# Performance work log

Hardware: AMD Instinct MI355X
Metric: run time of the kernel (lower is better)

The kernel has to match this reference:

```python
import jax, jax.numpy as jnp
import numpy as np

H, TD, NUM_NODES = 128, 32, 256
B, N, T = 16, 256, 128


def sinusoidal_pe(t, h, dtype=jnp.float32):
    pos = jnp.arange(t, dtype=dtype)[:, None]                      # [T,1]
    div = jnp.exp(jnp.arange(0, h, 2, dtype=dtype) * (-np.log(10000.0) / h))
    pe = jnp.zeros((t, h), dtype=dtype)
    pe = pe.at[:, 0::2].set(jnp.sin(pos * div))
    pe = pe.at[:, 1::2].set(jnp.cos(pos * div))
    return pe                                                      # [T,H]


def setup_inputs() -> dict:
    key = jax.random.key(0)
    ks = jax.random.split(key, 20)
    lin = lambda k, i, o: jax.random.normal(k, (i, o), jnp.float32) / np.sqrt(i)
    return {
        "xf": jax.random.normal(ks[0], (B, N, T, H), jnp.float32),
        "ex": jax.random.normal(ks[1], (B, T, TD), jnp.float32),
        "nf": jax.random.randint(ks[2], (N,), 0, NUM_NODES),
        "mask": jax.random.randint(ks[3], (B, N, T, H), 0, 2).astype(bool),
        "W_in": lin(ks[4], 3 * H, H), "b_in": jnp.zeros((H,), jnp.float32),
        "W_t": lin(ks[5], TD, H), "b_t": jnp.zeros((H,), jnp.float32),
        "E_node": jax.random.normal(ks[6], (NUM_NODES, H), jnp.float32),
        "W_q": lin(ks[7], H, H), "b_q": jnp.zeros((H,), jnp.float32),
        "W_k": lin(ks[8], H, H), "b_k": jnp.zeros((H,), jnp.float32),
        "W_v": lin(ks[9], H, H), "b_v": jnp.zeros((H,), jnp.float32),
        "W_o": lin(ks[10], H, H), "b_o": jnp.zeros((H,), jnp.float32),
    }


def reference(xf, ex, nf, mask, W_in, b_in, W_t, b_t, E_node,
              W_q, b_q, W_k, b_k, W_v, b_v, W_o, b_o):
    b, n, t, h = xf.shape
    # pos-embed + concat(time, node embeds) + linear + GELU (exact erf, like torch F.gelu)
    pe = sinusoidal_pe(t, h, xf.dtype)                              # [T,H]
    time_e = (ex @ W_t + b_t)[:, None, :, :]                        # [B,1,T,H]
    node_e = E_node[nf][None, :, None, :]                           # [1,N,1,H]
    cat = jnp.concatenate([
        xf + pe,
        jnp.broadcast_to(time_e, (b, n, t, h)),
        jnp.broadcast_to(node_e, (b, n, t, h)),
    ], axis=-1)                                                     # [B,N,T,3H]
    x = jax.nn.gelu(cat @ W_in + b_in, approximate=False)           # [B,N,T,H]
    # attention over T per (B,N)
    q = x @ W_q + b_q
    k = x @ W_k + b_k
    v = x @ W_v + b_v
    scores = jnp.einsum('bnsh,bnth->bnst', q, k) * (1.0 / np.sqrt(h))
    A = jnp.nan_to_num(jax.nn.softmax(scores, axis=-1), nan=0.0)    # [B,N,T,T]
    # masked-confidence reduction (detached A in original)
    t_masking = jnp.all(mask, axis=-1)[:, :, None, :].astype(A.dtype)  # [B,N,1,T]
    conf = 1.0 - jnp.sum(jax.lax.stop_gradient(A) * t_masking, axis=-1)  # [B,N,T]
    rec = jnp.einsum('bnst,bnth->bnsh', A, v)                       # [B,N,T,H]
    rec = rec @ W_o + b_o
    return rec, conf
```

## Files before the change

### kernel.cpp

```cpp
#include <hip/hip_runtime.h>
#include <hip/hip_bf16.h>
#include <stdint.h>


typedef __bf16 bf16;
typedef __bf16 bf16x4 __attribute__((ext_vector_type(4)));
typedef __bf16 bf16x8 __attribute__((ext_vector_type(8)));
typedef float  f32x4  __attribute__((ext_vector_type(4)));

#define MFMA16(a, b, c) __builtin_amdgcn_mfma_f32_16x16x32_bf16((a), (b), (c), 0, 0, 0)

__device__ __forceinline__ int allBytesNonzero(unsigned v) {
    return ((v - 0x01010101u) & ~v & 0x80808080u) == 0u;
}

__device__ __forceinline__ bf16x8 cvt8(const float* p) {
    float4 f0 = *reinterpret_cast<const float4*>(p);
    float4 f1 = *reinterpret_cast<const float4*>(p + 4);
    bf16x8 r;
    r[0] = (bf16)f0.x; r[1] = (bf16)f0.y; r[2] = (bf16)f0.z; r[3] = (bf16)f0.w;
    r[4] = (bf16)f1.x; r[5] = (bf16)f1.y; r[6] = (bf16)f1.z; r[7] = (bf16)f1.w;
    return r;
}

__device__ __forceinline__ float gelu_erf(float v) {
    float x  = v * 0.70710678118654752f;
    float ax = fabsf(x);
    float t  = __builtin_amdgcn_rcpf(1.0f + 0.3275911f * ax);
    float p  = ((((1.061405429f * t - 1.453152027f) * t + 1.421413741f) * t
                 - 0.284496736f) * t + 0.254829592f) * t;
    float er = 1.0f - p * __expf(-ax * ax);
    er = copysignf(er, x);
    return 0.5f * v * (1.0f + er);
}

__global__ void prep_all(const float* __restrict__ W_in, const float* __restrict__ Wq,
                         const float* __restrict__ Wk, const float* __restrict__ bq,
                         const float* __restrict__ Wv, const float* __restrict__ Wo,
                         const float* __restrict__ bv, const float* __restrict__ bo,
                         const int* __restrict__ nf, const float* __restrict__ E_node,
                         bf16* __restrict__ wsW, bf16* __restrict__ mstore,
                         bf16* __restrict__ nstore, float* __restrict__ vvec,
                         float* __restrict__ bias2, float* __restrict__ npart)
{
    const int blk = blockIdx.x, t = threadIdx.x;
    if (blk < 128) {
        wsW[blk * 128 + (t ^ ((blk & 15) << 3))] = (bf16)W_in[t * 128 + blk];
    } else if (blk < 256) {
        const int a = blk - 128;
        __shared__ float wqa[128];
        wqa[t] = Wq[a * 128 + t];
        __syncthreads();
        float acc = 0.f;
        for (int k = 0; k < 128; ++k) acc += wqa[k] * Wk[t * 128 + k];
        mstore[a * 128 + (t ^ ((a & 15) << 3))] = (bf16)acc;
        if (a == 0) {
            float av = 0.f;
            for (int j = 0; j < 128; ++j) av += Wk[t * 128 + j] * bq[j];
            vvec[t] = av;
        }
    } else if (blk < 384) {
        const int h = blk - 256;
        __shared__ float wvh[128];
        wvh[t] = Wv[h * 128 + t];
        __syncthreads();
        float acc = 0.f;
        for (int j = 0; j < 128; ++j) acc += wvh[j] * Wo[j * 128 + t];
        nstore[t * 128 + (h ^ ((t & 15) << 3))] = (bf16)acc;
        if (h == 0) {
            float b2 = 0.f;
            for (int j = 0; j < 128; ++j) b2 += bv[j] * Wo[j * 128 + t];
            bias2[t] = b2 + bo[t];
        }
    } else {
        const int n = blk - 384;
        int node = nf[n];
        const float* e = E_node + node * 128;
        float acc = 0.f;
        for (int k = 0; k < 128; ++k) acc += e[k] * W_in[(256 + k) * 128 + t];
        npart[n * 128 + t] = acc;
    }
}

__global__ void prep_bias(const float* __restrict__ ex, const float* __restrict__ W_t,
                          const float* __restrict__ b_t, const float* __restrict__ W_in,
                          const float* __restrict__ b_in, float* __restrict__ biasT)
{
    const int bt = blockIdx.x;
    const int t = bt & 127;
    const int h = threadIdx.x;
    __shared__ float te[128];
    __shared__ float sn[64], cs[64];
    float v = b_t[h];
    const float* exr = ex + (size_t)bt * 32;
    for (int d = 0; d < 32; ++d) v += exr[d] * W_t[d * 128 + h];
    te[h] = v;
    if (h < 64) {
        const float ninv = -9.210340371976184f / 128.0f;
        float div = expf((float)(2 * h) * ninv);
        float ang = (float)t * div;
        sn[h] = sinf(ang);
        cs[h] = cosf(ang);
    }
    __syncthreads();
    float acc = b_in[h];
    for (int j = 0; j < 64; ++j)
        acc += sn[j] * W_in[(2 * j) * 128 + h] + cs[j] * W_in[(2 * j + 1) * 128 + h];
    for (int k = 0; k < 128; ++k) acc += te[k] * W_in[(128 + k) * 128 + h];
    biasT[(size_t)bt * 128 + h] = acc;
}

#define STAGE_ISSUE(SRC)                                                        \
    {                                                                           \
        _Pragma("unroll")                                                       \
        for (int i = 0; i < 4; ++i)                                             \
            stg[i] = *reinterpret_cast<const bf16x8*>((SRC) + (tid + i * 512) * 8); \
    }
#define STAGE_WRITE()                                                           \
    {                                                                           \
        _Pragma("unroll")                                                       \
        for (int i = 0; i < 4; ++i)                                             \
            *reinterpret_cast<bf16x8*>(&sW[(tid + i * 512) * 8]) = stg[i];      \
    }

__global__ __launch_bounds__(512, 4) void fused_main(
    const float* __restrict__ xf, const unsigned char* __restrict__ mask,
    const bf16* __restrict__ wsW, const float* __restrict__ biasT,
    const float* __restrict__ npart, const float* __restrict__ vvec,
    const float* __restrict__ bias2, float* __restrict__ out)
{
    const bf16* W1T = wsW;
    const bf16* Mst = wsW + 16384;
    const bf16* Nst = wsW + 32768;

    __shared__ bf16 sW[16384];
    __shared__ bf16 sKV[128][136];
    __shared__ bf16 sT[8][16][40];
    __shared__ __align__(16) float sTm[128];
    __shared__ __align__(16) float sWt[128];

    const int bn = blockIdx.x;
    const int b  = bn >> 8;
    const int n  = bn & 255;
    const int tid  = (int)threadIdx.x;
    const int w    = tid >> 6;
    const int lane = tid & 63;
    const int c = lane & 15;
    const int g = lane >> 4;
    const int s0 = w << 4;

    const f32x4 FZ = {0.f, 0.f, 0.f, 0.f};
    bf16x8 stg[4];
    bf16* patch = &sT[w][0][0];

    if (tid < 128) {
        const uint4* mp = reinterpret_cast<const uint4*>(mask + ((size_t)bn * 128 + tid) * 128);
        int ok = 1;
        #pragma unroll
        for (int i = 0; i < 8; ++i) {
            uint4 u = mp[i];
            ok &= allBytesNonzero(u.x) & allBytesNonzero(u.y)
                & allBytesNonzero(u.z) & allBytesNonzero(u.w);
        }
        sTm[tid] = ok ? 1.0f : 0.0f;
    }

    STAGE_ISSUE(W1T);
    bf16x8 af[4];
    {
        const float* xfb = xf + (size_t)bn * 16384;
        #pragma unroll
        for (int kk = 0; kk < 4; ++kk)
            af[kk] = cvt8(xfb + (s0 + c) * 128 + kk * 32 + g * 8);
    }
    STAGE_WRITE();
    __syncthreads();

    STAGE_ISSUE(Mst);
    bf16x8 xb[4];
    {
        const float* biasB = biasT + (size_t)b * 16384;
        const float* npRow = npart + n * 128;
        const int t = s0 + c;
        float bbr[8][4];
        #pragma unroll
        for (int ht = 0; ht < 8; ++ht) {
            const int hb = ht * 16 + g * 4;
            const float4 bb  = *reinterpret_cast<const float4*>(biasB + t * 128 + hb);
            const float4 np4 = *reinterpret_cast<const float4*>(npRow + hb);
            bbr[ht][0] = bb.x + np4.x; bbr[ht][1] = bb.y + np4.y;
            bbr[ht][2] = bb.z + np4.z; bbr[ht][3] = bb.w + np4.w;
        }
        f32x4 acc[8];
        #pragma unroll
        for (int ht = 0; ht < 8; ++ht) acc[ht] = FZ;
        __builtin_amdgcn_s_setprio(1);
        #pragma unroll
        for (int kk = 0; kk < 4; ++kk) {
            const int k0 = kk * 32 + g * 8;
            #pragma unroll
            for (int ht = 0; ht < 8; ++ht) {
                bf16x8 aw = *reinterpret_cast<const bf16x8*>(
                    &sW[(ht * 16 + c) * 128 + (k0 ^ ((c & 15) << 3))]);
                acc[ht] = MFMA16(aw, af[kk], acc[ht]);
            }
        }
        __builtin_amdgcn_s_setprio(0);
        bf16x4 pk[8];
        #pragma unroll
        for (int ht = 0; ht < 8; ++ht)
            #pragma unroll
            for (int r = 0; r < 4; ++r)
                pk[ht][r] = (bf16)gelu_erf(acc[ht][r] + bbr[ht][r]);
        #pragma unroll
        for (int kk = 0; kk < 4; ++kk) {
            *reinterpret_cast<bf16x4*>(patch + c * 40 + g * 4)      = pk[2 * kk];
            *reinterpret_cast<bf16x4*>(patch + c * 40 + 16 + g * 4) = pk[2 * kk + 1];
            xb[kk] = *reinterpret_cast<const bf16x8*>(patch + c * 40 + g * 8);
        }
    }
    __syncthreads();

    STAGE_WRITE();
    __syncthreads();

    STAGE_ISSUE(Nst);
    {
        f32x4 acc[8];
        #pragma unroll
        for (int ht = 0; ht < 8; ++ht) acc[ht] = FZ;
        __builtin_amdgcn_s_setprio(1);
        #pragma unroll
        for (int kk = 0; kk < 4; ++kk) {
            const int k0 = kk * 32 + g * 8;
            #pragma unroll
            for (int ht = 0; ht < 8; ++ht) {
                bf16x8 aw = *reinterpret_cast<const bf16x8*>(
                    &sW[(ht * 16 + c) * 128 + (k0 ^ ((c & 15) << 3))]);
                acc[ht] = MFMA16(aw, xb[kk], acc[ht]);
            }
        }
        __builtin_amdgcn_s_setprio(0);
        const int t = s0 + c;
        #pragma unroll
        for (int ht = 0; ht < 8; ++ht) {
            bf16x4 pk;
            #pragma unroll
            for (int r = 0; r < 4; ++r) pk[r] = (bf16)acc[ht][r];
            *reinterpret_cast<bf16x4*>(&sKV[t][ht * 16 + g * 4]) = pk;
        }
        float wd = 0.f;
        #pragma unroll
        for (int kk = 0; kk < 4; ++kk) {
            const float4 vA = *reinterpret_cast<const float4*>(vvec + kk * 32 + g * 8);
            const float4 vB = *reinterpret_cast<const float4*>(vvec + kk * 32 + g * 8 + 4);
            wd += (float)xb[kk][0] * vA.x + (float)xb[kk][1] * vA.y
                + (float)xb[kk][2] * vA.z + (float)xb[kk][3] * vA.w
                + (float)xb[kk][4] * vB.x + (float)xb[kk][5] * vB.y
                + (float)xb[kk][6] * vB.z + (float)xb[kk][7] * vB.w;
        }
        wd += __shfl_xor(wd, 16);
        wd += __shfl_xor(wd, 32);
        if (g == 0) sWt[t] = wd;
    }
    __syncthreads();

    STAGE_WRITE();
    __syncthreads();

    const float rs = 0.08838834764831845f;
    float invl = 1.f;
    bf16x8 xp[4];
    bf16x4 vpk[8];

    {
        f32x4 sc[8];
        #pragma unroll
        for (int rt = 0; rt < 8; ++rt) sc[rt] = FZ;
        __builtin_amdgcn_s_setprio(1);
        #pragma unroll
        for (int kk = 0; kk < 4; ++kk) {
            const int k0 = kk * 32 + g * 8;
            #pragma unroll
            for (int rt = 0; rt < 8; ++rt) {
                bf16x8 ay = *reinterpret_cast<const bf16x8*>(&sKV[rt * 16 + c][k0]);
                sc[rt] = MFMA16(ay, xb[kk], sc[rt]);
            }
        }
        __builtin_amdgcn_s_setprio(0);

        {
            f32x4 acc[8];
            #pragma unroll
            for (int ct = 0; ct < 8; ++ct) acc[ct] = FZ;
            __builtin_amdgcn_s_setprio(1);
            #pragma unroll
            for (int kk = 0; kk < 4; ++kk) {
                const int k0 = kk * 32 + g * 8;
                #pragma unroll
                for (int ct = 0; ct < 8; ++ct) {
                    bf16x8 bw = *reinterpret_cast<const bf16x8*>(
                        &sW[(ct * 16 + c) * 128 + (k0 ^ ((c & 15) << 3))]);
                    acc[ct] = MFMA16(xb[kk], bw, acc[ct]);
                }
            }
            __builtin_amdgcn_s_setprio(0);
            #pragma unroll
            for (int ct = 0; ct < 8; ++ct)
                #pragma unroll
                for (int r = 0; r < 4; ++r)
                    vpk[ct][r] = (bf16)acc[ct][r];
        }

        float ls = 0.f, wsum = 0.f;
        #pragma unroll
        for (int rt = 0; rt < 8; ++rt) {
            const float4 wt4 = *reinterpret_cast<const float4*>(&sWt[rt * 16 + g * 4]);
            const float4 tm4 = *reinterpret_cast<const float4*>(&sTm[rt * 16 + g * 4]);
            const float wtr[4] = {wt4.x, wt4.y, wt4.z, wt4.w};
            const float tmr[4] = {tm4.x, tm4.y, tm4.z, tm4.w};
            #pragma unroll
            for (int r = 0; r < 4; ++r) {
                float p = __expf((sc[rt][r] + wtr[r]) * rs);
                sc[rt][r] = p;
                ls += p;
                wsum += p * tmr[r];
            }
        }
        ls   += __shfl_xor(ls, 16);   ls   += __shfl_xor(ls, 32);
        wsum += __shfl_xor(wsum, 16); wsum += __shfl_xor(wsum, 32);
        invl = __builtin_amdgcn_rcpf(ls);
        if (g == 0)
            out[(size_t)67108864 + (size_t)bn * 128 + s0 + c] = 1.0f - wsum * invl;
        bf16x4 pkP[8];
        #pragma unroll
        for (int rt = 0; rt < 8; ++rt)
            #pragma unroll
            for (int r = 0; r < 4; ++r) pkP[rt][r] = (bf16)sc[rt][r];
        #pragma unroll
        for (int kk = 0; kk < 4; ++kk) {
            *reinterpret_cast<bf16x4*>(patch + c * 40 + g * 4)      = pkP[2 * kk];
            *reinterpret_cast<bf16x4*>(patch + c * 40 + 16 + g * 4) = pkP[2 * kk + 1];
            xp[kk] = *reinterpret_cast<const bf16x8*>(patch + c * 40 + g * 8);
        }
    }
    __syncthreads();

    {
        #pragma unroll
        for (int ct = 0; ct < 8; ++ct)
            *reinterpret_cast<bf16x4*>(&sKV[ct * 16 + c][s0 + g * 4]) = vpk[ct];
    }
    __syncthreads();

    {
        f32x4 rc[8];
        #pragma unroll
        for (int rt = 0; rt < 8; ++rt) rc[rt] = FZ;
        __builtin_amdgcn_s_setprio(1);
        #pragma unroll
        for (int kk = 0; kk < 4; ++kk) {
            const int k0 = kk * 32 + g * 8;
            #pragma unroll
            for (int rt = 0; rt < 8; ++rt) {
                bf16x8 avf = *reinterpret_cast<const bf16x8*>(&sKV[rt * 16 + c][k0]);
                rc[rt] = MFMA16(avf, xp[kk], rc[rt]);
            }
        }
        __builtin_amdgcn_s_setprio(0);
        float* outb = out + (size_t)bn * 16384 + (size_t)(s0 + c) * 128;
        #pragma unroll
        for (int rt = 0; rt < 8; ++rt) {
            const int hb = rt * 16 + g * 4;
            const float4 b2 = *reinterpret_cast<const float4*>(bias2 + hb);
            float4 v;
            v.x = rc[rt][0] * invl + b2.x;
            v.y = rc[rt][1] * invl + b2.y;
            v.z = rc[rt][2] * invl + b2.z;
            v.w = rc[rt][3] * invl + b2.w;
            *reinterpret_cast<float4*>(outb + hb) = v;
        }
    }
}

extern "C" void kernel_launch(void* const* d_in, const int* in_sizes, int n_in,
                              void* d_out, int out_size, void* d_ws, size_t ws_size,
                              hipStream_t stream)
{
    (void)in_sizes; (void)n_in; (void)out_size; (void)ws_size;
    const float* xf     = (const float*)d_in[0];
    const float* ex     = (const float*)d_in[1];
    const int*   nf     = (const int*)d_in[2];
    const unsigned char* mask = (const unsigned char*)d_in[3];
    const float* W_in   = (const float*)d_in[4];
    const float* b_in   = (const float*)d_in[5];
    const float* W_t    = (const float*)d_in[6];
    const float* b_t    = (const float*)d_in[7];
    const float* E_node = (const float*)d_in[8];
    const float* W_q    = (const float*)d_in[9];
    const float* b_q    = (const float*)d_in[10];
    const float* W_k    = (const float*)d_in[11];
    const float* b_k    = (const float*)d_in[12];
    const float* W_v    = (const float*)d_in[13];
    const float* b_v    = (const float*)d_in[14];
    const float* W_o    = (const float*)d_in[15];
    const float* b_o    = (const float*)d_in[16];
    (void)b_k;
    float* out = (float*)d_out;

    bf16*  wsW    = (bf16*)d_ws;
    bf16*  mstore = wsW + 16384;
    bf16*  nstore = wsW + 32768;
    float* biasT  = (float*)((char*)d_ws + 98304);
    float* npart  = (float*)((char*)d_ws + 1146880);
    float* vvec   = (float*)((char*)d_ws + 1277952);
    float* bias2  = (float*)((char*)d_ws + 1278464);

    prep_all<<<640, 128, 0, stream>>>(W_in, W_q, W_k, b_q, W_v, W_o, b_v, b_o,
                                      nf, E_node, wsW, mstore, nstore,
                                      vvec, bias2, npart);
    prep_bias<<<2048, 128, 0, stream>>>(ex, W_t, b_t, W_in, b_in, biasT);
    fused_main<<<4096, 512, 0, stream>>>(xf, mask, wsW, biasT, npart,
                                         vvec, bias2, out);
}
```

Before: 224.8 us.

## Halve block to 256 threads, each wave computing two 16-row tiles

The fused kernel now runs 4 waves per block instead of 8, and each wave handles 32 query rows as two 16-row subtiles. Every weight/K/V fragment read from LDS feeds two MFMAs, which halves LDS fragment traffic per MFMA. The V projection is also reordered ahead of the score computation. In exchange, register pressure roughly doubles for accumulators, and launch bounds drop to 2 blocks per CU, so occupancy and latency hiding may fall.

```diff
diff --git a/kernel.cpp b/kernel.cpp
--- a/kernel.cpp
+++ b/kernel.cpp
@@ -113,17 +113,17 @@
 #define STAGE_ISSUE(SRC)                                                        \
     {                                                                           \
         _Pragma("unroll")                                                       \
-        for (int i = 0; i < 4; ++i)                                             \
-            stg[i] = *reinterpret_cast<const bf16x8*>((SRC) + (tid + i * 512) * 8); \
+        for (int i = 0; i < 8; ++i)                                             \
+            stg[i] = *reinterpret_cast<const bf16x8*>((SRC) + (tid + i * 256) * 8); \
     }
 #define STAGE_WRITE()                                                           \
     {                                                                           \
         _Pragma("unroll")                                                       \
-        for (int i = 0; i < 4; ++i)                                             \
-            *reinterpret_cast<bf16x8*>(&sW[(tid + i * 512) * 8]) = stg[i];      \
-    }
-
-__global__ __launch_bounds__(512, 4) void fused_main(
+        for (int i = 0; i < 8; ++i)                                             \
+            *reinterpret_cast<bf16x8*>(&sW[(tid + i * 256) * 8]) = stg[i];      \
+    }
+
+__global__ __launch_bounds__(256, 2) void fused_main(
     const float* __restrict__ xf, const unsigned char* __restrict__ mask,
     const bf16* __restrict__ wsW, const float* __restrict__ biasT,
     const float* __restrict__ npart, const float* __restrict__ vvec,
@@ -135,7 +135,7 @@
 
     __shared__ bf16 sW[16384];
     __shared__ bf16 sKV[128][136];
-    __shared__ bf16 sT[8][16][40];
+    __shared__ bf16 sT[4][16][40];
     __shared__ __align__(16) float sTm[128];
     __shared__ __align__(16) float sWt[128];
 
@@ -147,10 +147,10 @@
     const int lane = tid & 63;
     const int c = lane & 15;
     const int g = lane >> 4;
-    const int s0 = w << 4;
+    const int s0 = w << 5;
 
     const f32x4 FZ = {0.f, 0.f, 0.f, 0.f};
-    bf16x8 stg[4];
+    bf16x8 stg[8];
     bf16* patch = &sT[w][0][0];
 
     if (tid < 128) {
@@ -166,34 +166,28 @@
     }
 
     STAGE_ISSUE(W1T);
-    bf16x8 af[4];
+    bf16x8 af[2][4];
     {
         const float* xfb = xf + (size_t)bn * 16384;
         #pragma unroll
-        for (int kk = 0; kk < 4; ++kk)
-            af[kk] = cvt8(xfb + (s0 + c) * 128 + kk * 32 + g * 8);
+        for (int st = 0; st < 2; ++st)
+            #pragma unroll
+            for (int kk = 0; kk < 4; ++kk)
+                af[st][kk] = cvt8(xfb + (s0 + st * 16 + c) * 128 + kk * 32 + g * 8);
     }
     STAGE_WRITE();
     __syncthreads();
 
     STAGE_ISSUE(Mst);
-    bf16x8 xb[4];
+    bf16x8 xb[2][4];
     {
         const float* biasB = biasT + (size_t)b * 16384;
         const float* npRow = npart + n * 128;
-        const int t = s0 + c;
-        float bbr[8][4];
-        #pragma unroll
-        for (int ht = 0; ht < 8; ++ht) {
-            const int hb = ht * 16 + g * 4;
-            const float4 bb  = *reinterpret_cast<const float4*>(biasB + t * 128 + hb);
-            const float4 np4 = *reinterpret_cast<const float4*>(npRow + hb);
-            bbr[ht][0] = bb.x + np4.x; bbr[ht][1] = bb.y + np4.y;
-            bbr[ht][2] = bb.z + np4.z; bbr[ht][3] = bb.w + np4.w;
-        }
-        f32x4 acc[8];
-        #pragma unroll
-        for (int ht = 0; ht < 8; ++ht) acc[ht] = FZ;
+        f32x4 acc[2][8];
+        #pragma unroll
+        for (int st = 0; st < 2; ++st)
+            #pragma unroll
+            for (int ht = 0; ht < 8; ++ht) acc[st][ht] = FZ;
         __builtin_amdgcn_s_setprio(1);
         #pragma unroll
         for (int kk = 0; kk < 4; ++kk) {
@@ -202,21 +196,31 @@
             for (int ht = 0; ht < 8; ++ht) {
                 bf16x8 aw = *reinterpret_cast<const bf16x8*>(
                     &sW[(ht * 16 + c) * 128 + (k0 ^ ((c & 15) << 3))]);
-                acc[ht] = MFMA16(aw, af[kk], acc[ht]);
+                acc[0][ht] = MFMA16(aw, af[0][kk], acc[0][ht]);
+                acc[1][ht] = MFMA16(aw, af[1][kk], acc[1][ht]);
             }
         }
         __builtin_amdgcn_s_setprio(0);
-        bf16x4 pk[8];
-        #pragma unroll
-        for (int ht = 0; ht < 8; ++ht)
-            #pragma unroll
-            for (int r = 0; r < 4; ++r)
-                pk[ht][r] = (bf16)gelu_erf(acc[ht][r] + bbr[ht][r]);
-        #pragma unroll
-        for (int kk = 0; kk < 4; ++kk) {
-            *reinterpret_cast<bf16x4*>(patch + c * 40 + g * 4)      = pk[2 * kk];
-            *reinterpret_cast<bf16x4*>(patch + c * 40 + 16 + g * 4) = pk[2 * kk + 1];
-            xb[kk] = *reinterpret_cast<const bf16x8*>(patch + c * 40 + g * 8);
+        #pragma unroll
+        for (int st = 0; st < 2; ++st) {
+            const int t = s0 + st * 16 + c;
+            bf16x4 pk[8];
+            #pragma unroll
+            for (int ht = 0; ht < 8; ++ht) {
+                const int hb = ht * 16 + g * 4;
+                const float4 bb  = *reinterpret_cast<const float4*>(biasB + t * 128 + hb);
+                const float4 np4 = *reinterpret_cast<const float4*>(npRow + hb);
+                pk[ht][0] = (bf16)gelu_erf(acc[st][ht][0] + bb.x + np4.x);
+                pk[ht][1] = (bf16)gelu_erf(acc[st][ht][1] + bb.y + np4.y);
+                pk[ht][2] = (bf16)gelu_erf(acc[st][ht][2] + bb.z + np4.z);
+                pk[ht][3] = (bf16)gelu_erf(acc[st][ht][3] + bb.w + np4.w);
+            }
+            #pragma unroll
+            for (int kk = 0; kk < 4; ++kk) {
+                *reinterpret_cast<bf16x4*>(patch + c * 40 + g * 4)      = pk[2 * kk];
+                *reinterpret_cast<bf16x4*>(patch + c * 40 + 16 + g * 4) = pk[2 * kk + 1];
+                xb[st][kk] = *reinterpret_cast<const bf16x8*>(patch + c * 40 + g * 8);
+            }
         }
     }
     __syncthreads();
@@ -226,9 +230,11 @@
 
     STAGE_ISSUE(Nst);
     {
-        f32x4 acc[8];
-        #pragma unroll
-        for (int ht = 0; ht < 8; ++ht) acc[ht] = FZ;
+        f32x4 acc[2][8];
+        #pragma unroll
+        for (int st = 0; st < 2; ++st)
+            #pragma unroll
+            for (int ht = 0; ht < 8; ++ht) acc[st][ht] = FZ;
         __builtin_amdgcn_s_setprio(1);
         #pragma unroll
         for (int kk = 0; kk < 4; ++kk) {
@@ -237,31 +243,35 @@
             for (int ht = 0; ht < 8; ++ht) {
                 bf16x8 aw = *reinterpret_cast<const bf16x8*>(
                     &sW[(ht * 16 + c) * 128 + (k0 ^ ((c & 15) << 3))]);
-                acc[ht] = MFMA16(aw, xb[kk], acc[ht]);
+                acc[0][ht] = MFMA16(aw, xb[0][kk], acc[0][ht]);
+                acc[1][ht] = MFMA16(aw, xb[1][kk], acc[1][ht]);
             }
         }
         __builtin_amdgcn_s_setprio(0);
-        const int t = s0 + c;
-        #pragma unroll
-        for (int ht = 0; ht < 8; ++ht) {
-            bf16x4 pk;
-            #pragma unroll
-            for (int r = 0; r < 4; ++r) pk[r] = (bf16)acc[ht][r];
-            *reinterpret_cast<bf16x4*>(&sKV[t][ht * 16 + g * 4]) = pk;
-        }
-        float wd = 0.f;
-        #pragma unroll
-        for (int kk = 0; kk < 4; ++kk) {
-            const float4 vA = *reinterpret_cast<const float4*>(vvec + kk * 32 + g * 8);
-            const float4 vB = *reinterpret_cast<const float4*>(vvec + kk * 32 + g * 8 + 4);
-            wd += (float)xb[kk][0] * vA.x + (float)xb[kk][1] * vA.y
-                + (float)xb[kk][2] * vA.z + (float)xb[kk][3] * vA.w
-                + (float)xb[kk][4] * vB.x + (float)xb[kk][5] * vB.y
-                + (float)xb[kk][6] * vB.z + (float)xb[kk][7] * vB.w;
-        }
-        wd += __shfl_xor(wd, 16);
-        wd += __shfl_xor(wd, 32);
-        if (g == 0) sWt[t] = wd;
+        #pragma unroll
+        for (int st = 0; st < 2; ++st) {
+            const int t = s0 + st * 16 + c;
+            #pragma unroll
+            for (int ht = 0; ht < 8; ++ht) {
+                bf16x4 pk;
+                #pragma unroll
+                for (int r = 0; r < 4; ++r) pk[r] = (bf16)acc[st][ht][r];
+                *reinterpret_cast<bf16x4*>(&sKV[t][ht * 16 + g * 4]) = pk;
+            }
+            float wd = 0.f;
+            #pragma unroll
+            for (int kk = 0; kk < 4; ++kk) {
+                const float4 vA = *reinterpret_cast<const float4*>(vvec + kk * 32 + g * 8);
+                const float4 vB = *reinterpret_cast<const float4*>(vvec + kk * 32 + g * 8 + 4);
+                wd += (float)xb[st][kk][0] * vA.x + (float)xb[st][kk][1] * vA.y
+                    + (float)xb[st][kk][2] * vA.z + (float)xb[st][kk][3] * vA.w
+                    + (float)xb[st][kk][4] * vB.x + (float)xb[st][kk][5] * vB.y
+                    + (float)xb[st][kk][6] * vB.z + (float)xb[st][kk][7] * vB.w;
+            }
+            wd += __shfl_xor(wd, 16);
+            wd += __shfl_xor(wd, 32);
+            if (g == 0) sWt[t] = wd;
+        }
     }
     __syncthreads();
 
@@ -269,116 +279,137 @@
     __syncthreads();
 
     const float rs = 0.08838834764831845f;
-    float invl = 1.f;
-    bf16x8 xp[4];
-    bf16x4 vpk[8];
-
-    {
-        f32x4 sc[8];
-        #pragma unroll
-        for (int rt = 0; rt < 8; ++rt) sc[rt] = FZ;
+    float invl[2] = {1.f, 1.f};
+    bf16x8 xp[2][4];
+    bf16x4 vpk[2][8];
+
+    {
+        f32x4 acc[2][8];
+        #pragma unroll
+        for (int st = 0; st < 2; ++st)
+            #pragma unroll
+            for (int ct = 0; ct < 8; ++ct) acc[st][ct] = FZ;
         __builtin_amdgcn_s_setprio(1);
         #pragma unroll
         for (int kk = 0; kk < 4; ++kk) {
             const int k0 = kk * 32 + g * 8;
             #pragma unroll
-            for (int rt = 0; rt < 8; ++rt) {
-                bf16x8 ay = *reinterpret_cast<const bf16x8*>(&sKV[rt * 16 + c][k0]);
-                sc[rt] = MFMA16(ay, xb[kk], sc[rt]);
+            for (int ct = 0; ct < 8; ++ct) {
+                bf16x8 bw = *reinterpret_cast<const bf16x8*>(
+                    &sW[(ct * 16 + c) * 128 + (k0 ^ ((c & 15) << 3))]);
+                acc[0][ct] = MFMA16(xb[0][kk], bw, acc[0][ct]);
+                acc[1][ct] = MFMA16(xb[1][kk], bw, acc[1][ct]);
             }
         }
         __builtin_amdgcn_s_setprio(0);
-
-        {
-            f32x4 acc[8];
-            #pragma unroll
-            for (int ct = 0; ct < 8; ++ct) acc[ct] = FZ;
-            __builtin_amdgcn_s_setprio(1);
-            #pragma unroll
-            for (int kk = 0; kk < 4; ++kk) {
-                const int k0 = kk * 32 + g * 8;
-                #pragma unroll
-                for (int ct = 0; ct < 8; ++ct) {
-                    bf16x8 bw = *reinterpret_cast<const bf16x8*>(
-                        &sW[(ct * 16 + c) * 128 + (k0 ^ ((c & 15) << 3))]);
-                    acc[ct] = MFMA16(xb[kk], bw, acc[ct]);
-                }
-            }
-            __builtin_amdgcn_s_setprio(0);
+        #pragma unroll
+        for (int st = 0; st < 2; ++st)
             #pragma unroll
             for (int ct = 0; ct < 8; ++ct)
                 #pragma unroll
                 for (int r = 0; r < 4; ++r)
-                    vpk[ct][r] = (bf16)acc[ct][r];
-        }
-
-        float ls = 0.f, wsum = 0.f;
-        #pragma unroll
-        for (int rt = 0; rt < 8; ++rt) {
-            const float4 wt4 = *reinterpret_cast<const float4*>(&sWt[rt * 16 + g * 4]);
-            const float4 tm4 = *reinterpret_cast<const float4*>(&sTm[rt * 16 + g * 4]);
-            const float wtr[4] = {wt4.x, wt4.y, wt4.z, wt4.w};
-            const float tmr[4] = {tm4.x, tm4.y, tm4.z, tm4.w};
-            #pragma unroll
-            for (int r = 0; r < 4; ++r) {
-                float p = __expf((sc[rt][r] + wtr[r]) * rs);
-                sc[rt][r] = p;
-                ls += p;
-                wsum += p * tmr[r];
-            }
-        }
-        ls   += __shfl_xor(ls, 16);   ls   += __shfl_xor(ls, 32);
-        wsum += __shfl_xor(wsum, 16); wsum += __shfl_xor(wsum, 32);
-        invl = __builtin_amdgcn_rcpf(ls);
-        if (g == 0)
-            out[(size_t)67108864 + (size_t)bn * 128 + s0 + c] = 1.0f - wsum * invl;
-        bf16x4 pkP[8];
-        #pragma unroll
-        for (int rt = 0; rt < 8; ++rt)
-            #pragma unroll
-            for (int r = 0; r < 4; ++r) pkP[rt][r] = (bf16)sc[rt][r];
-        #pragma unroll
-        for (int kk = 0; kk < 4; ++kk) {
-            *reinterpret_cast<bf16x4*>(patch + c * 40 + g * 4)      = pkP[2 * kk];
-            *reinterpret_cast<bf16x4*>(patch + c * 40 + 16 + g * 4) = pkP[2 * kk + 1];
-            xp[kk] = *reinterpret_cast<const bf16x8*>(patch + c * 40 + g * 8);
-        }
-    }
-    __syncthreads();
-
-    {
-        #pragma unroll
-        for (int ct = 0; ct < 8; ++ct)
-            *reinterpret_cast<bf16x4*>(&sKV[ct * 16 + c][s0 + g * 4]) = vpk[ct];
-    }
-    __syncthreads();
-
-    {
-        f32x4 rc[8];
-        #pragma unroll
-        for (int rt = 0; rt < 8; ++rt) rc[rt] = FZ;
+                    vpk[st][ct][r] = (bf16)acc[st][ct][r];
+    }
+
+    {
+        f32x4 sc[2][8];
+        #pragma unroll
+        for (int st = 0; st < 2; ++st)
+            #pragma unroll
+            for (int rt = 0; rt < 8; ++rt) sc[st][rt] = FZ;
         __builtin_amdgcn_s_setprio(1);
         #pragma unroll
         for (int kk = 0; kk < 4; ++kk) {
             const int k0 = kk * 32 + g * 8;
             #pragma unroll
             for (int rt = 0; rt < 8; ++rt) {
+                bf16x8 ay = *reinterpret_cast<const bf16x8*>(&sKV[rt * 16 + c][k0]);
+                sc[0][rt] = MFMA16(ay, xb[0][kk], sc[0][rt]);
+                sc[1][rt] = MFMA16(ay, xb[1][kk], sc[1][rt]);
+            }
+        }
+        __builtin_amdgcn_s_setprio(0);
+
+        #pragma unroll
+        for (int st = 0; st < 2; ++st) {
+            float ls = 0.f, wsum = 0.f;
+            #pragma unroll
+            for (int rt = 0; rt < 8; ++rt) {
+                const float4 wt4 = *reinterpret_cast<const float4*>(&sWt[rt * 16 + g * 4]);
+                const float4 tm4 = *reinterpret_cast<const float4*>(&sTm[rt * 16 + g * 4]);
+                const float wtr[4] = {wt4.x, wt4.y, wt4.z, wt4.w};
+                const float tmr[4] = {tm4.x, tm4.y, tm4.z, tm4.w};
+                #pragma unroll
+                for (int r = 0; r < 4; ++r) {
+                    float p = __expf((sc[st][rt][r] + wtr[r]) * rs);
+                    sc[st][rt][r] = p;
+                    ls += p;
+                    wsum += p * tmr[r];
+                }
+            }
+            ls   += __shfl_xor(ls, 16);   ls   += __shfl_xor(ls, 32);
+            wsum += __shfl_xor(wsum, 16); wsum += __shfl_xor(wsum, 32);
+            invl[st] = __builtin_amdgcn_rcpf(ls);
+            if (g == 0)
+                out[(size_t)67108864 + (size_t)bn * 128 + s0 + st * 16 + c]
+                    = 1.0f - wsum * invl[st];
+            bf16x4 pkP[8];
+            #pragma unroll
+            for (int rt = 0; rt < 8; ++rt)
+                #pragma unroll
+                for (int r = 0; r < 4; ++r) pkP[rt][r] = (bf16)sc[st][rt][r];
+            #pragma unroll
+            for (int kk = 0; kk < 4; ++kk) {
+                *reinterpret_cast<bf16x4*>(patch + c * 40 + g * 4)      = pkP[2 * kk];
+                *reinterpret_cast<bf16x4*>(patch + c * 40 + 16 + g * 4) = pkP[2 * kk + 1];
+                xp[st][kk] = *reinterpret_cast<const bf16x8*>(patch + c * 40 + g * 8);
+            }
+        }
+    }
+    __syncthreads();
+
+    {
+        #pragma unroll
+        for (int st = 0; st < 2; ++st)
+            #pragma unroll
+            for (int ct = 0; ct < 8; ++ct)
+                *reinterpret_cast<bf16x4*>(&sKV[ct * 16 + c][s0 + st * 16 + g * 4]) = vpk[st][ct];
+    }
+    __syncthreads();
+
+    {
+        f32x4 rc[2][8];
+        #pragma unroll
+        for (int st = 0; st < 2; ++st)
+            #pragma unroll
+            for (int rt = 0; rt < 8; ++rt) rc[st][rt] = FZ;
+        __builtin_amdgcn_s_setprio(1);
+        #pragma unroll
+        for (int kk = 0; kk < 4; ++kk) {
+            const int k0 = kk * 32 + g * 8;
+            #pragma unroll
+            for (int rt = 0; rt < 8; ++rt) {
                 bf16x8 avf = *reinterpret_cast<const bf16x8*>(&sKV[rt * 16 + c][k0]);
-                rc[rt] = MFMA16(avf, xp[kk], rc[rt]);
+                rc[0][rt] = MFMA16(avf, xp[0][kk], rc[0][rt]);
+                rc[1][rt] = MFMA16(avf, xp[1][kk], rc[1][rt]);
             }
         }
         __builtin_amdgcn_s_setprio(0);
-        float* outb = out + (size_t)bn * 16384 + (size_t)(s0 + c) * 128;
-        #pragma unroll
-        for (int rt = 0; rt < 8; ++rt) {
-            const int hb = rt * 16 + g * 4;
-            const float4 b2 = *reinterpret_cast<const float4*>(bias2 + hb);
-            float4 v;
-            v.x = rc[rt][0] * invl + b2.x;
-            v.y = rc[rt][1] * invl + b2.y;
-            v.z = rc[rt][2] * invl + b2.z;
-            v.w = rc[rt][3] * invl + b2.w;
-            *reinterpret_cast<float4*>(outb + hb) = v;
+        #pragma unroll
+        for (int st = 0; st < 2; ++st) {
+            float* outb = out + (size_t)bn * 16384 + (size_t)(s0 + st * 16 + c) * 128;
+            const float il = invl[st];
+            #pragma unroll
+            for (int rt = 0; rt < 8; ++rt) {
+                const int hb = rt * 16 + g * 4;
+                const float4 b2 = *reinterpret_cast<const float4*>(bias2 + hb);
+                float4 v;
+                v.x = rc[st][rt][0] * il + b2.x;
+                v.y = rc[st][rt][1] * il + b2.y;
+                v.z = rc[st][rt][2] * il + b2.z;
+                v.w = rc[st][rt][3] * il + b2.w;
+                *reinterpret_cast<float4*>(outb + hb) = v;
+            }
         }
     }
 }
@@ -420,6 +451,6 @@
                                       nf, E_node, wsW, mstore, nstore,
                                       vvec, bias2, npart);
     prep_bias<<<2048, 128, 0, stream>>>(ex, W_t, b_t, W_in, b_in, biasT);
-    fused_main<<<4096, 512, 0, stream>>>(xf, mask, wsW, biasT, npart,
+    fused_main<<<4096, 256, 0, stream>>>(xf, mask, wsW, biasT, npart,
                                          vvec, bias2, out);
 }
```

Measured after the change: 241.4 us, median of 2. +7.4%, slower.

## Double-buffer weight staging in LDS and move V projection after softmax

Applied to the files above, without the earlier changes.

Replaces the single weight buffer and padded K/V buffer with two 32 KB LDS buffers. The first two weight matrices are prefetched together, which removes one staging write and two barriers. The V-projection GEMM moves to after the softmax barrier so it can read its weights from the second buffer. The K/V tile now uses an XOR-swizzled unpadded layout instead of padding. The cost is more LDS per block, which may lower occupancy, and more live staging registers.

```diff
diff --git a/kernel.cpp b/kernel.cpp
--- a/kernel.cpp
+++ b/kernel.cpp
@@ -110,17 +110,17 @@
     biasT[(size_t)bt * 128 + h] = acc;
 }
 
-#define STAGE_ISSUE(SRC)                                                        \
+#define STAGE_ISSUE(REGS, SRC)                                                  \
     {                                                                           \
         _Pragma("unroll")                                                       \
         for (int i = 0; i < 4; ++i)                                             \
-            stg[i] = *reinterpret_cast<const bf16x8*>((SRC) + (tid + i * 512) * 8); \
-    }
-#define STAGE_WRITE()                                                           \
+            REGS[i] = *reinterpret_cast<const bf16x8*>((SRC) + (tid + i * 512) * 8); \
+    }
+#define STAGE_WRITE(REGS, DST)                                                  \
     {                                                                           \
         _Pragma("unroll")                                                       \
         for (int i = 0; i < 4; ++i)                                             \
-            *reinterpret_cast<bf16x8*>(&sW[(tid + i * 512) * 8]) = stg[i];      \
+            *reinterpret_cast<bf16x8*>(&(DST)[(tid + i * 512) * 8]) = REGS[i];  \
     }
 
 __global__ __launch_bounds__(512, 4) void fused_main(
@@ -133,8 +133,8 @@
     const bf16* Mst = wsW + 16384;
     const bf16* Nst = wsW + 32768;
 
-    __shared__ bf16 sW[16384];
-    __shared__ bf16 sKV[128][136];
+    __shared__ bf16 sA[16384];
+    __shared__ bf16 sB[16384];
     __shared__ bf16 sT[8][16][40];
     __shared__ __align__(16) float sTm[128];
     __shared__ __align__(16) float sWt[128];
@@ -150,8 +150,9 @@
     const int s0 = w << 4;
 
     const f32x4 FZ = {0.f, 0.f, 0.f, 0.f};
-    bf16x8 stg[4];
+    bf16x8 stgA[4], stgB[4];
     bf16* patch = &sT[w][0][0];
+    const int cx = c << 3;
 
     if (tid < 128) {
         const uint4* mp = reinterpret_cast<const uint4*>(mask + ((size_t)bn * 128 + tid) * 128);
@@ -165,7 +166,8 @@
         sTm[tid] = ok ? 1.0f : 0.0f;
     }
 
-    STAGE_ISSUE(W1T);
+    STAGE_ISSUE(stgA, W1T);
+    STAGE_ISSUE(stgB, Mst);
     bf16x8 af[4];
     {
         const float* xfb = xf + (size_t)bn * 16384;
@@ -173,10 +175,10 @@
         for (int kk = 0; kk < 4; ++kk)
             af[kk] = cvt8(xfb + (s0 + c) * 128 + kk * 32 + g * 8);
     }
-    STAGE_WRITE();
-    __syncthreads();
-
-    STAGE_ISSUE(Mst);
+    STAGE_WRITE(stgA, sA);
+    STAGE_WRITE(stgB, sB);
+    __syncthreads();
+
     bf16x8 xb[4];
     {
         const float* biasB = biasT + (size_t)b * 16384;
@@ -201,7 +203,7 @@
             #pragma unroll
             for (int ht = 0; ht < 8; ++ht) {
                 bf16x8 aw = *reinterpret_cast<const bf16x8*>(
-                    &sW[(ht * 16 + c) * 128 + (k0 ^ ((c & 15) << 3))]);
+                    &sA[(ht * 16 + c) * 128 + (k0 ^ cx)]);
                 acc[ht] = MFMA16(aw, af[kk], acc[ht]);
             }
         }
@@ -221,10 +223,7 @@
     }
     __syncthreads();
 
-    STAGE_WRITE();
-    __syncthreads();
-
-    STAGE_ISSUE(Nst);
+    STAGE_ISSUE(stgA, Nst);
     {
         f32x4 acc[8];
         #pragma unroll
@@ -236,7 +235,7 @@
             #pragma unroll
             for (int ht = 0; ht < 8; ++ht) {
                 bf16x8 aw = *reinterpret_cast<const bf16x8*>(
-                    &sW[(ht * 16 + c) * 128 + (k0 ^ ((c & 15) << 3))]);
+                    &sB[(ht * 16 + c) * 128 + (k0 ^ cx)]);
                 acc[ht] = MFMA16(aw, xb[kk], acc[ht]);
             }
         }
@@ -247,7 +246,7 @@
             bf16x4 pk;
             #pragma unroll
             for (int r = 0; r < 4; ++r) pk[r] = (bf16)acc[ht][r];
-            *reinterpret_cast<bf16x4*>(&sKV[t][ht * 16 + g * 4]) = pk;
+            *reinterpret_cast<bf16x4*>(&sA[t * 128 + ((ht * 16 + g * 4) ^ cx)]) = pk;
         }
         float wd = 0.f;
         #pragma unroll
@@ -265,13 +264,9 @@
     }
     __syncthreads();
 
-    STAGE_WRITE();
-    __syncthreads();
-
     const float rs = 0.08838834764831845f;
     float invl = 1.f;
     bf16x8 xp[4];
-    bf16x4 vpk[8];
 
     {
         f32x4 sc[8];
@@ -283,34 +278,14 @@
             const int k0 = kk * 32 + g * 8;
             #pragma unroll
             for (int rt = 0; rt < 8; ++rt) {
-                bf16x8 ay = *reinterpret_cast<const bf16x8*>(&sKV[rt * 16 + c][k0]);
+                bf16x8 ay = *reinterpret_cast<const bf16x8*>(
+                    &sA[(rt * 16 + c) * 128 + (k0 ^ cx)]);
                 sc[rt] = MFMA16(ay, xb[kk], sc[rt]);
             }
         }
         __builtin_amdgcn_s_setprio(0);
 
-        {
-            f32x4 acc[8];
-            #pragma unroll
-            for (int ct = 0; ct < 8; ++ct) acc[ct] = FZ;
-            __builtin_amdgcn_s_setprio(1);
-            #pragma unroll
-            for (int kk = 0; kk < 4; ++kk) {
-                const int k0 = kk * 32 + g * 8;
-                #pragma unroll
-                for (int ct = 0; ct < 8; ++ct) {
-                    bf16x8 bw = *reinterpret_cast<const bf16x8*>(
-                        &sW[(ct * 16 + c) * 128 + (k0 ^ ((c & 15) << 3))]);
-                    acc[ct] = MFMA16(xb[kk], bw, acc[ct]);
-                }
-            }
-            __builtin_amdgcn_s_setprio(0);
-            #pragma unroll
-            for (int ct = 0; ct < 8; ++ct)
-                #pragma unroll
-                for (int r = 0; r < 4; ++r)
-                    vpk[ct][r] = (bf16)acc[ct][r];
-        }
+        STAGE_WRITE(stgA, sB);
 
         float ls = 0.f, wsum = 0.f;
         #pragma unroll
@@ -347,9 +322,28 @@
     __syncthreads();
 
     {
-        #pragma unroll
-        for (int ct = 0; ct < 8; ++ct)
-            *reinterpret_cast<bf16x4*>(&sKV[ct * 16 + c][s0 + g * 4]) = vpk[ct];
+        f32x4 acc[8];
+        #pragma unroll
+        for (int ct = 0; ct < 8; ++ct) acc[ct] = FZ;
+        __builtin_amdgcn_s_setprio(1);
+        #pragma unroll
+        for (int kk = 0; kk < 4; ++kk) {
+            const int k0 = kk * 32 + g * 8;
+            #pragma unroll
+            for (int ct = 0; ct < 8; ++ct) {
+                bf16x8 bw = *reinterpret_cast<const bf16x8*>(
+                    &sB[(ct * 16 + c) * 128 + (k0 ^ cx)]);
+                acc[ct] = MFMA16(xb[kk], bw, acc[ct]);
+            }
+        }
+        __builtin_amdgcn_s_setprio(0);
+        #pragma unroll
+        for (int ct = 0; ct < 8; ++ct) {
+            bf16x4 pk;
+            #pragma unroll
+            for (int r = 0; r < 4; ++r) pk[r] = (bf16)acc[ct][r];
+            *reinterpret_cast<bf16x4*>(&sA[(ct * 16 + c) * 128 + ((s0 + g * 4) ^ cx)]) = pk;
+        }
     }
     __syncthreads();
 
@@ -363,7 +357,8 @@
             const int k0 = kk * 32 + g * 8;
             #pragma unroll
             for (int rt = 0; rt < 8; ++rt) {
-                bf16x8 avf = *reinterpret_cast<const bf16x8*>(&sKV[rt * 16 + c][k0]);
+                bf16x8 avf = *reinterpret_cast<const bf16x8*>(
+                    &sA[(rt * 16 + c) * 128 + (k0 ^ cx)]);
                 rc[rt] = MFMA16(avf, xp[kk], rc[rt]);
             }
         }
```

Measured after the change: 225.0 us. Within noise of the previous version (+0.1%).
